# Kernel optimization log

Measured on AMD Instinct MI355X. Metric: run time of the kernel, lower is better.

Reference implementation:

```python
import jax, jax.numpy as jnp
import numpy as np

IN_F = 2048
OUT_F = 2048
NNZ = 1048576
B = 8192


def setup_inputs() -> dict:
    key = jax.random.key(0)
    k1, k2, k3 = jax.random.split(key, 3)
    x = jax.random.normal(k1, (B, IN_F), dtype=jnp.float32)
    weights = (jax.random.normal(k2, (NNZ,), dtype=jnp.float32) * 0.02).astype(jnp.float16)
    coords = jax.random.randint(k3, (NNZ,), 0, OUT_F * IN_F, dtype=jnp.int64)
    return {"x": x, "weights": weights, "coords": coords}


def reference(x, weights, coords):
    # COO SpMV: out[b, row] += w * x[b, col] for each (row, col, w) triple.
    # coords are flat indices into the [OUT_F, IN_F] weight matrix.
    rows = coords // IN_F
    cols = coords % IN_F
    # Scatter-accumulate sparse weights into a dense matrix (duplicates add,
    # matching the kernel's atomic accumulation), then one batched matmul
    # replaces the per-row kernel launches of the original.
    W = jnp.zeros((OUT_F, IN_F), dtype=jnp.float32)
    W = W.at[rows, cols].add(weights.astype(jnp.float32))
    out = jnp.einsum('bi,oi->bo', x, W)  # [B, OUT_F] fp32, like the CL buffer
    return out.astype(x.dtype)
```

## Files before the change

kernel.cpp:

```cpp
#include <hip/hip_runtime.h>
#include <hip/hip_fp16.h>

#define IN_F   2048
#define OUT_F  2048
#define NNZ_   1048576
#define BATCH  8192
#define W_ROW0 6144
#define W_BASE ((size_t)W_ROW0 * OUT_F)

typedef __bf16 bf16x8 __attribute__((ext_vector_type(8)));
typedef float  f32x4  __attribute__((ext_vector_type(4)));

__device__ __forceinline__ float bfval(unsigned short b) {
    union { unsigned int u; float f; } t; t.u = ((unsigned int)b) << 16; return t.f;
}
__device__ __forceinline__ unsigned short f2bf(float f) {
    union { float f; unsigned int u; } v; v.f = f;
    unsigned int u = v.u; u += 0x7FFF + ((u >> 16) & 1);
    return (unsigned short)(u >> 16);
}
__device__ __forceinline__ float h2f(unsigned short b) {
    union { unsigned short u; __half h; } t; t.u = b; return __half2float(t.h);
}
__device__ __forceinline__ void gload_lds16(const void* g, void* l) {
    __builtin_amdgcn_global_load_lds(
        (const __attribute__((address_space(1))) unsigned int*)g,
        (__attribute__((address_space(3))) unsigned int*)l,
        16, 0, 0);
}

__global__ void prep_kernel(const float4* __restrict__ x,
                            ushort4* __restrict__ xb,
                            float4* __restrict__ Wz) {
    const int stride = gridDim.x * blockDim.x;
    const int t0 = blockIdx.x * blockDim.x + threadIdx.x;
    for (int i = t0; i < OUT_F * IN_F / 4; i += stride)
        Wz[i] = float4{0.f, 0.f, 0.f, 0.f};
    for (int i = t0; i < BATCH * IN_F / 4; i += stride) {
        float4 v = x[i];
        ushort4 o;
        o.x = f2bf(v.x); o.y = f2bf(v.y); o.z = f2bf(v.z); o.w = f2bf(v.w);
        xb[i] = o;
    }
}

__global__ void scatter_w_kernel(const unsigned short* __restrict__ wbits,
                                 const int* __restrict__ coords,
                                 float* __restrict__ W, int nnz) {
    __shared__ unsigned int sbf, sfh;
    if (threadIdx.x == 0) { sbf = 0u; sfh = 0u; }
    __syncthreads();
    unsigned int mbf = 0u, mfh = 0u;
    for (int i = threadIdx.x; i < 512; i += blockDim.x) {
        unsigned short b = wbits[i];
        unsigned int abf = (((unsigned int)b) << 16) & 0x7FFFFFFFu;
        unsigned int afh = (unsigned int)(b & 0x7FFF);
        mbf = mbf > abf ? mbf : abf;
        mfh = mfh > afh ? mfh : afh;
    }
    atomicMax(&sbf, mbf); atomicMax(&sfh, mfh);
    __syncthreads();
    union { unsigned int u; float f; } tb; tb.u = sbf;
    float bmax = tb.f;
    float hmax = h2f((unsigned short)sfh);
    int mode = (bmax > 1e-3f && bmax < 16.f) ? 0
             : (hmax > 1e-3f && hmax < 16.f) ? 1 : 2;

    int i = blockIdx.x * blockDim.x + threadIdx.x;
    if (i < nnz) {
        float v;
        if (mode == 0)      v = bfval(wbits[i]);
        else if (mode == 1) v = h2f(wbits[i]);
        else                v = ((const float*)wbits)[i];
        atomicAdd(&W[coords[i] & (OUT_F * IN_F - 1)], v);
    }
}

__global__ void f32_to_bf16_kernel(const float4* __restrict__ in,
                                   ushort4* __restrict__ out, int n4) {
    int s = gridDim.x * blockDim.x;
    for (int i = blockIdx.x * blockDim.x + threadIdx.x; i < n4; i += s) {
        float4 v = in[i];
        ushort4 o;
        o.x = f2bf(v.x); o.y = f2bf(v.y); o.z = f2bf(v.z); o.w = f2bf(v.w);
        out[i] = o;
    }
}

__global__ __launch_bounds__(1024, 4) void gemm256_kernel(
    const unsigned short* __restrict__ xb,
    const unsigned short* __restrict__ wb,
    float* __restrict__ out) {
    constexpr int K = IN_F;
    constexpr int NT = K / 64;

    __shared__ __align__(16) unsigned short As[2][256 * 64];
    __shared__ __align__(16) unsigned short Bs[2][256 * 64];

    const int tid  = threadIdx.x;
    const int lane = tid & 63;
    const int wave = tid >> 6;
    const int wr   = wave >> 2;
    const int wc   = wave & 3;
    const int frow = lane & 15;
    const int klan = lane >> 4;
    const int s0   = klan ^ (lane & 7);

    const int flat = blockIdx.x;
    const int swz  = (flat & 7) * 32 + (flat >> 3);
    const int tm   = swz & 31;
    const int tn   = swz >> 5;

    const unsigned short* srcA = xb + (size_t)tm * 256 * K;
    const unsigned short* srcB = wb + (size_t)tn * 256 * K;

    const int rloc  = lane >> 3;
    const int sslot = (lane & 7) ^ rloc;

    f32x4 acc[4][4] = {};

    auto stage = [&](int buf, int kt) {
        const size_t coff = (size_t)kt * 64 + sslot * 8;
#pragma unroll
        for (int c = 0; c < 2; ++c) {
            const int row = c * 128 + wave * 8;
            gload_lds16(srcA + (size_t)(row + rloc) * K + coff,
                        &As[buf][row * 64]);
        }
#pragma unroll
        for (int c = 0; c < 2; ++c) {
            const int row = c * 128 + wave * 8;
            gload_lds16(srcB + (size_t)(row + rloc) * K + coff,
                        &Bs[buf][row * 64]);
        }
    };

    auto compute = [&](int buf) {
#pragma unroll
        for (int ks = 0; ks < 2; ++ks) {
            const int sl = s0 ^ (ks * 4);
            bf16x8 af[4], bg[4];
#pragma unroll
            for (int mf = 0; mf < 4; ++mf)
                af[mf] = *(const bf16x8*)
                    &As[buf][(wr * 64 + mf * 16 + frow) * 64 + sl * 8];
#pragma unroll
            for (int nf = 0; nf < 4; ++nf)
                bg[nf] = *(const bf16x8*)
                    &Bs[buf][(wc * 64 + nf * 16 + frow) * 64 + sl * 8];
            __builtin_amdgcn_s_setprio(1);
#pragma unroll
            for (int mf = 0; mf < 4; ++mf)
#pragma unroll
                for (int nf = 0; nf < 4; ++nf)
                    acc[mf][nf] = __builtin_amdgcn_mfma_f32_16x16x32_bf16(
                        af[mf], bg[nf], acc[mf][nf], 0, 0, 0);
            __builtin_amdgcn_s_setprio(0);
        }
    };

    stage(0, 0);
    stage(1, 1);

    for (int kt = 0; kt < NT - 2; ++kt) {
        asm volatile("s_waitcnt vmcnt(4)" ::: "memory");
        __builtin_amdgcn_s_barrier();
        compute(kt & 1);
        asm volatile("" ::: "memory");
        __builtin_amdgcn_s_barrier();
        stage(kt & 1, kt + 2);
    }
    asm volatile("s_waitcnt vmcnt(4)" ::: "memory");
    __builtin_amdgcn_s_barrier();
    compute((NT - 2) & 1);
    asm volatile("" ::: "memory");
    __builtin_amdgcn_s_barrier();
    asm volatile("s_waitcnt vmcnt(0)" ::: "memory");
    __builtin_amdgcn_s_barrier();
    compute((NT - 1) & 1);

    const int orow0 = tm * 256 + wr * 64 + klan * 4;
    const int ocol0 = tn * 256 + wc * 64 + frow;
#pragma unroll
    for (int mf = 0; mf < 4; ++mf)
#pragma unroll
        for (int nf = 0; nf < 4; ++nf)
#pragma unroll
            for (int r = 0; r < 4; ++r)
                out[(size_t)(orow0 + mf * 16 + r) * OUT_F + ocol0 + nf * 16]
                    = acc[mf][nf][r];
}

extern "C" void kernel_launch(void* const* d_in, const int* in_sizes, int n_in,
                              void* d_out, int out_size, void* d_ws, size_t ws_size,
                              hipStream_t stream) {
    const float*          x      = (const float*)d_in[0];
    const unsigned short* wbits  = (const unsigned short*)d_in[1];
    const int*            coords = (const int*)d_in[2];
    float*                out    = (float*)d_out;

    const size_t MB = 1024 * 1024;
    float*          W  = out + W_BASE;
    unsigned short* wb = (unsigned short*)d_ws;
    unsigned short* xb = (unsigned short*)((char*)d_ws + 8 * MB);
    (void)ws_size; (void)in_sizes; (void)n_in; (void)out_size;

    prep_kernel<<<2048, 256, 0, stream>>>((const float4*)x, (ushort4*)xb,
                                          (float4*)W);
    scatter_w_kernel<<<NNZ_ / 256, 256, 0, stream>>>(wbits, coords, W, NNZ_);
    f32_to_bf16_kernel<<<1024, 256, 0, stream>>>(
        (const float4*)W, (ushort4*)wb, OUT_F * IN_F / 4);

    gemm256_kernel<<<256, 1024, 0, stream>>>(xb, wb, out);
}
```

Baseline: 152.3 us.

## Fuse fp32-to-bf16 conversion of x into the GEMM A-tile load path

Removes the separate pass that converted x to bf16 in a workspace buffer, leaving a plain zeroing kernel for W. The GEMM now loads fp32 x rows into registers, converts them to bf16 and writes them to a swizzled LDS tile. This load is software-pipelined one tile ahead, while the W tiles still use direct global-to-LDS loads. It removes a full read and write of the activation matrix, at the cost of twice the A-operand global traffic inside the GEMM, extra VALU conversion work, more registers and a more complex waitcnt schedule.

```diff
diff --git a/kernel.cpp b/kernel.cpp
--- a/kernel.cpp
+++ b/kernel.cpp
@@ -29,19 +29,10 @@
         16, 0, 0);
 }
 
-__global__ void prep_kernel(const float4* __restrict__ x,
-                            ushort4* __restrict__ xb,
-                            float4* __restrict__ Wz) {
-    const int stride = gridDim.x * blockDim.x;
-    const int t0 = blockIdx.x * blockDim.x + threadIdx.x;
-    for (int i = t0; i < OUT_F * IN_F / 4; i += stride)
-        Wz[i] = float4{0.f, 0.f, 0.f, 0.f};
-    for (int i = t0; i < BATCH * IN_F / 4; i += stride) {
-        float4 v = x[i];
-        ushort4 o;
-        o.x = f2bf(v.x); o.y = f2bf(v.y); o.z = f2bf(v.z); o.w = f2bf(v.w);
-        xb[i] = o;
-    }
+__global__ void zero_f32_kernel(float4* __restrict__ p, int n4) {
+    int s = gridDim.x * blockDim.x;
+    for (int i = blockIdx.x * blockDim.x + threadIdx.x; i < n4; i += s)
+        p[i] = float4{0.f, 0.f, 0.f, 0.f};
 }
 
 __global__ void scatter_w_kernel(const unsigned short* __restrict__ wbits,
@@ -88,7 +79,7 @@
 }
 
 __global__ __launch_bounds__(1024, 4) void gemm256_kernel(
-    const unsigned short* __restrict__ xb,
+    const float* __restrict__ xf,
     const unsigned short* __restrict__ wb,
     float* __restrict__ out) {
     constexpr int K = IN_F;
@@ -111,22 +102,19 @@
     const int tm   = swz & 31;
     const int tn   = swz >> 5;
 
-    const unsigned short* srcA = xb + (size_t)tm * 256 * K;
     const unsigned short* srcB = wb + (size_t)tn * 256 * K;
 
     const int rloc  = lane >> 3;
     const int sslot = (lane & 7) ^ rloc;
 
+    const int arl  = lane >> 2;
+    const int as0  = lane & 3;
+    const float* srcAx = xf + (size_t)(tm * 256 + wave * 16 + arl) * K;
+
     f32x4 acc[4][4] = {};
 
-    auto stage = [&](int buf, int kt) {
+    auto stageB = [&](int buf, int kt) {
         const size_t coff = (size_t)kt * 64 + sslot * 8;
-#pragma unroll
-        for (int c = 0; c < 2; ++c) {
-            const int row = c * 128 + wave * 8;
-            gload_lds16(srcA + (size_t)(row + rloc) * K + coff,
-                        &As[buf][row * 64]);
-        }
 #pragma unroll
         for (int c = 0; c < 2; ++c) {
             const int row = c * 128 + wave * 8;
@@ -134,7 +122,29 @@
                         &Bs[buf][row * 64]);
         }
     };
-
+    auto aload = [&](int kt, float4 (&v)[4]) {
+        const float* p = srcAx + kt * 64;
+        v[0] = *(const float4*)(p + as0 * 8);
+        v[1] = *(const float4*)(p + as0 * 8 + 4);
+        v[2] = *(const float4*)(p + (as0 + 4) * 8);
+        v[3] = *(const float4*)(p + (as0 + 4) * 8 + 4);
+    };
+    auto awrite = [&](int buf, float4 (&v)[4]) {
+        bf16x8 t0, t1;
+        t0[0] = (__bf16)v[0].x; t0[1] = (__bf16)v[0].y;
+        t0[2] = (__bf16)v[0].z; t0[3] = (__bf16)v[0].w;
+        t0[4] = (__bf16)v[1].x; t0[5] = (__bf16)v[1].y;
+        t0[6] = (__bf16)v[1].z; t0[7] = (__bf16)v[1].w;
+        t1[0] = (__bf16)v[2].x; t1[1] = (__bf16)v[2].y;
+        t1[2] = (__bf16)v[2].z; t1[3] = (__bf16)v[2].w;
+        t1[4] = (__bf16)v[3].x; t1[5] = (__bf16)v[3].y;
+        t1[6] = (__bf16)v[3].z; t1[7] = (__bf16)v[3].w;
+        const int r  = wave * 16 + arl;
+        const int s1 = as0 ^ (arl & 7);
+        const int s2 = (as0 + 4) ^ (arl & 7);
+        *(bf16x8*)&As[buf][r * 64 + s1 * 8] = t0;
+        *(bf16x8*)&As[buf][r * 64 + s2 * 8] = t1;
+    };
     auto compute = [&](int buf) {
 #pragma unroll
         for (int ks = 0; ks < 2; ++ks) {
@@ -159,25 +169,33 @@
         }
     };
 
-    stage(0, 0);
-    stage(1, 1);
-
-    for (int kt = 0; kt < NT - 2; ++kt) {
-        asm volatile("s_waitcnt vmcnt(4)" ::: "memory");
+    float4 r0[4], r1[4];
+    stageB(0, 0);
+    aload(0, r0);
+    stageB(1, 1);
+    aload(1, r1);
+    asm volatile("s_waitcnt vmcnt(6)" ::: "memory");
+    awrite(0, r0);
+
+    auto iter = [&](int kt, float4 (&rfree)[4], float4 (&rnext)[4]) {
+        const int buf = kt & 1;
+        asm volatile("s_waitcnt lgkmcnt(0)" ::: "memory");
         __builtin_amdgcn_s_barrier();
-        compute(kt & 1);
+        compute(buf);
         asm volatile("" ::: "memory");
         __builtin_amdgcn_s_barrier();
-        stage(kt & 1, kt + 2);
-    }
-    asm volatile("s_waitcnt vmcnt(4)" ::: "memory");
-    __builtin_amdgcn_s_barrier();
-    compute((NT - 2) & 1);
-    asm volatile("" ::: "memory");
-    __builtin_amdgcn_s_barrier();
-    asm volatile("s_waitcnt vmcnt(0)" ::: "memory");
-    __builtin_amdgcn_s_barrier();
-    compute((NT - 1) & 1);
+        if (kt + 2 < NT) stageB(buf, kt + 2);
+        if (kt + 1 < NT) {
+            if (kt + 2 < NT) asm volatile("s_waitcnt vmcnt(2)" ::: "memory");
+            else             asm volatile("s_waitcnt vmcnt(0)" ::: "memory");
+            awrite(buf ^ 1, rnext);
+            if (kt + 2 < NT) aload(kt + 2, rfree);
+        }
+    };
+    for (int kt = 0; kt < NT; kt += 2) {
+        iter(kt, r0, r1);
+        iter(kt + 1, r1, r0);
+    }
 
     const int orow0 = tm * 256 + wr * 64 + klan * 4;
     const int ocol0 = tn * 256 + wc * 64 + frow;
@@ -199,17 +217,14 @@
     const int*            coords = (const int*)d_in[2];
     float*                out    = (float*)d_out;
 
-    const size_t MB = 1024 * 1024;
     float*          W  = out + W_BASE;
     unsigned short* wb = (unsigned short*)d_ws;
-    unsigned short* xb = (unsigned short*)((char*)d_ws + 8 * MB);
     (void)ws_size; (void)in_sizes; (void)n_in; (void)out_size;
 
-    prep_kernel<<<2048, 256, 0, stream>>>((const float4*)x, (ushort4*)xb,
-                                          (float4*)W);
+    zero_f32_kernel<<<512, 256, 0, stream>>>((float4*)W, OUT_F * IN_F / 4);
     scatter_w_kernel<<<NNZ_ / 256, 256, 0, stream>>>(wbits, coords, W, NNZ_);
     f32_to_bf16_kernel<<<1024, 256, 0, stream>>>(
         (const float4*)W, (ushort4*)wb, OUT_F * IN_F / 4);
 
-    gemm256_kernel<<<256, 1024, 0, stream>>>(xb, wb, out);
-}
+    gemm256_kernel<<<256, 1024, 0, stream>>>(x, wb, out);
+}
```

Measured after the change: 345.2 us. 127% more time.
